# Kernel tuning notes

Hardware: AMD Instinct MI355X
Metric: run time of the kernel (lower is better)

The kernel has to match this reference:

```python
import jax, jax.numpy as jnp
import numpy as np

# regular 3x3 kernel grid: row0 = dy (i-1), row1 = dx (j-1), k = 3*i + j
RY = jnp.array([-1., -1., -1., 0., 0., 0., 1., 1., 1.], dtype=jnp.float32)
RX = jnp.array([-1., 0., 1., -1., 0., 1., -1., 0., 1.], dtype=jnp.float32)


def conv2d(x, w, b):
    # 3x3, stride 1, pad 1, NCHW/OIHW
    out = jax.lax.conv_general_dilated(
        x, w, window_strides=(1, 1), padding=((1, 1), (1, 1)),
        dimension_numbers=('NCHW', 'OIHW', 'NCHW'))
    return out + b[None, :, None, None]


def group_norm(x, gamma, beta, num_groups, eps=1e-5):
    N, C, H, W = x.shape
    xg = x.reshape(N, num_groups, C // num_groups, H, W)
    mu = xg.mean(axis=(2, 3, 4), keepdims=True)
    var = xg.var(axis=(2, 3, 4), keepdims=True)
    xn = ((xg - mu) * jax.lax.rsqrt(var + eps)).reshape(N, C, H, W)
    return xn * gamma[None, :, None, None] + beta[None, :, None, None]


def build_offset(tm, tr):
    # tm: [N,4,H,W] per-pixel 2x2 affine [[m00,m01],[m10,m11]]; tr: [N,2,H,W] (ty, tx)
    m00, m01, m10, m11 = tm[:, 0], tm[:, 1], tm[:, 2], tm[:, 3]  # [N,H,W]
    ry = RY[None, :, None, None]
    rx = RX[None, :, None, None]
    # offset = M @ R - R, plus translation broadcast to all 9 points
    dy = m00[:, None] * ry + m01[:, None] * rx - ry + tr[:, 0:1]  # [N,9,H,W]
    dx = m10[:, None] * ry + m11[:, None] * rx - rx + tr[:, 1:2]  # [N,9,H,W]
    return dy, dx


def bilinear_sample(img, py, px):
    # img: [N,C,H,W]; py, px: [N,K,H,W] sampling locations; zero padding outside
    N, C, H, W = img.shape
    K = py.shape[1]
    y0f = jnp.floor(py)
    x0f = jnp.floor(px)
    wy1 = py - y0f
    wx1 = px - x0f
    wy0 = 1.0 - wy1
    wx0 = 1.0 - wx1
    y0 = y0f.astype(jnp.int32)
    x0 = x0f.astype(jnp.int32)
    img_flat = img.reshape(N, C, H * W)

    def gather(yi, xi):
        valid = ((yi >= 0) & (yi < H) & (xi >= 0) & (xi < W)).astype(img.dtype)
        idx = jnp.clip(yi, 0, H - 1) * W + jnp.clip(xi, 0, W - 1)  # [N,K,H,W]
        flat = idx.reshape(N, 1, K * H * W)
        vals = jnp.take_along_axis(img_flat, jnp.broadcast_to(flat, (N, C, K * H * W)), axis=2)
        return vals.reshape(N, C, K, H, W) * valid[:, None]

    v00 = gather(y0, x0)
    v01 = gather(y0, x0 + 1)
    v10 = gather(y0 + 1, x0)
    v11 = gather(y0 + 1, x0 + 1)
    return (v00 * (wy0 * wx0)[:, None] + v01 * (wy0 * wx1)[:, None]
            + v10 * (wy1 * wx0)[:, None] + v11 * (wy1 * wx1)[:, None])


def deform_conv(x, dy, dx, w, pad=1, dil=1):
    # x: [N,Cin,H,W]; dy,dx: [N,9,H,W]; w: [Cout,Cin,3,3]; stride 1
    N, C, H, W = x.shape
    k = jnp.arange(9)
    ki = (k // 3).astype(x.dtype)[None, :, None, None]
    kj = (k % 3).astype(x.dtype)[None, :, None, None]
    hh = jnp.arange(H, dtype=x.dtype)[None, None, :, None]
    ww = jnp.arange(W, dtype=x.dtype)[None, None, None, :]
    py = hh - pad + dil * ki + dy  # [N,9,H,W]
    px = ww - pad + dil * kj + dx
    sampled = bilinear_sample(x, py, px)  # [N,C,9,H,W]
    return jnp.einsum('nckhw,ock->nohw', sampled, w.reshape(w.shape[0], C, 9))


def setup_inputs() -> dict:
    key = jax.random.key(0)
    ks = jax.random.split(key, 16)
    N, C, H, W = 4, 256, 64, 64
    x = jax.random.normal(ks[0], (N, C, H, W), jnp.float32)
    def p(k, shape, s):
        return jax.random.normal(k, shape, jnp.float32) * s
    s_off = 0.01                       # small STN heads -> modest offsets
    s_dc = 1.0 / np.sqrt(C * 9.0)      # deform-conv fan-in init
    return {
        'x': x,
        'w_tm1': p(ks[1], (4, C, 3, 3), s_off), 'b_tm1': jnp.zeros((4,), jnp.float32),
        'w_tr1': p(ks[2], (2, C, 3, 3), s_off), 'b_tr1': jnp.zeros((2,), jnp.float32),
        'w_dc1': p(ks[3], (C, C, 3, 3), s_dc),
        'g1': jnp.ones((C,), jnp.float32), 'be1': jnp.zeros((C,), jnp.float32),
        'w_tm2': p(ks[4], (4, C, 3, 3), s_off), 'b_tm2': jnp.zeros((4,), jnp.float32),
        'w_tr2': p(ks[5], (2, C, 3, 3), s_off), 'b_tr2': jnp.zeros((2,), jnp.float32),
        'w_dc2': p(ks[6], (C, C, 3, 3), s_dc),
        'g2': jnp.ones((C,), jnp.float32), 'be2': jnp.zeros((C,), jnp.float32),
    }


def reference(x, w_tm1, b_tm1, w_tr1, b_tr1, w_dc1, g1, be1,
              w_tm2, b_tm2, w_tr2, b_tr2, w_dc2, g2, be2):
    GROUPS = 32
    residual = x
    dy1, dx1 = build_offset(conv2d(x, w_tm1, b_tm1), conv2d(x, w_tr1, b_tr1))
    out = deform_conv(x, dy1, dx1, w_dc1)
    out = jax.nn.relu(group_norm(out, g1, be1, GROUPS))
    dy2, dx2 = build_offset(conv2d(out, w_tm2, b_tm2), conv2d(out, w_tr2, b_tr2))
    out = deform_conv(out, dy2, dx2, w_dc2)
    out = group_norm(out, g2, be2, GROUPS)
    return jax.nn.relu(out + residual)
```

## Files before the change

### kernel.cpp

```cpp
#include <hip/hip_runtime.h>


typedef unsigned int u32;
typedef unsigned short u16;
typedef __attribute__((ext_vector_type(8))) short bf16x8;
typedef __attribute__((ext_vector_type(4))) float floatx4;

#define HW 4096
#define CHW 1048576

static __device__ __forceinline__ float bf2f(u16 u) {
    union { u32 i; float f; } c; c.i = ((u32)u) << 16; return c.f;
}
static __device__ __forceinline__ u16 f2bf(float f) {
    union { float f; u32 i; } c; c.f = f;
    u32 x = c.i;
    return (u16)((x + 0x7FFFu + ((x >> 16) & 1u)) >> 16);
}
static __device__ __forceinline__ float loadv(const void* p, long i, int f32) {
    return f32 ? ((const float*)p)[i] : bf2f(((const u16*)p)[i]);
}
static __device__ __forceinline__ int sniff_f32(const u32* __restrict__ xw) {
    int cnt = 0;
    #pragma unroll
    for (int s = 0; s < 16; ++s) {
        union { u32 i; float f; } c;
        c.i = xw[s * 131 + 7];
        float a = fabsf(c.f);
        if (a > 1e-8f && a < 1e4f) ++cnt;
    }
    return (cnt >= 8) ? 1 : 0;
}

__global__ __launch_bounds__(256) void k_prep_all(
    const void* __restrict__ x,
    const void* __restrict__ wdc1, const void* __restrict__ wdc2,
    const void* __restrict__ wtm1, const void* __restrict__ wtr1,
    const void* __restrict__ wtm2, const void* __restrict__ wtr2,
    u16* __restrict__ xT, u16* __restrict__ wTg1, u16* __restrict__ wTg2,
    u16* __restrict__ wT61, u16* __restrict__ wT62)
{
    __shared__ u16 T[64 * 258];
    const int f32 = sniff_f32((const u32*)x);
    const int b = blockIdx.x;
    const int tid = threadIdx.x;

    if (b < 256) {
        const int n = b >> 6, h = b & 63;
        const long sb = (long)n * CHW + (h << 6);
        const int cb = tid >> 3;
        const int w0 = (tid & 7) << 3;
        if (f32) {
            const float* xp = (const float*)x;
            for (int it = 0; it < 8; ++it) {
                int c = (it << 5) + cb;
                const float* pr = xp + sb + (long)c * HW + w0;
                float4 a = ((const float4*)pr)[0];
                float4 d = ((const float4*)pr)[1];
                T[(w0 + 0) * 258 + c] = f2bf(a.x);
                T[(w0 + 1) * 258 + c] = f2bf(a.y);
                T[(w0 + 2) * 258 + c] = f2bf(a.z);
                T[(w0 + 3) * 258 + c] = f2bf(a.w);
                T[(w0 + 4) * 258 + c] = f2bf(d.x);
                T[(w0 + 5) * 258 + c] = f2bf(d.y);
                T[(w0 + 6) * 258 + c] = f2bf(d.z);
                T[(w0 + 7) * 258 + c] = f2bf(d.w);
            }
        } else {
            const u16* xp = (const u16*)x;
            for (int it = 0; it < 8; ++it) {
                int c = (it << 5) + cb;
                uint4 v = *(const uint4*)(xp + sb + (long)c * HW + w0);
                u32 ws[4] = {v.x, v.y, v.z, v.w};
                #pragma unroll
                for (int q = 0; q < 4; ++q) {
                    T[(w0 + 2 * q + 0) * 258 + c] = (u16)(ws[q] & 0xFFFFu);
                    T[(w0 + 2 * q + 1) * 258 + c] = (u16)(ws[q] >> 16);
                }
            }
        }
        __syncthreads();
        const int w = tid >> 2, cq = tid & 3;
        const u32* Tr = (const u32*)T;
        u16* ob = xT + (long)n * CHW + (long)((h << 6) + w) * 256 + cq * 64;
        #pragma unroll
        for (int s = 0; s < 8; ++s) {
            uint4 o;
            o.x = Tr[129 * w + 32 * cq + 4 * s + 0];
            o.y = Tr[129 * w + 32 * cq + 4 * s + 1];
            o.z = Tr[129 * w + 32 * cq + 4 * s + 2];
            o.w = Tr[129 * w + 32 * cq + 4 * s + 3];
            *(uint4*)&ob[s * 8] = o;
        }
    } else if (b < 2560) {
        const int r2 = (b >= 1408);
        const void* wdc = r2 ? wdc2 : wdc1;
        u16* wTg = r2 ? wTg2 : wTg1;
        int idx2 = (b - (r2 ? 1408 : 256)) * 256 + tid;
        int cp = idx2 & 15;
        int o  = (idx2 >> 4) & 255;
        int q  = idx2 >> 12;
        int k  = q >> 3;
        int c0 = ((q & 7) << 5) + (cp << 1);
        long s0 = (long)o * 2304 + c0 * 9 + k;
        u16 w0 = f2bf(loadv(wdc, s0, f32));
        u16 w1 = f2bf(loadv(wdc, s0 + 9, f32));
        ((u32*)wTg)[idx2] = (u32)w0 | ((u32)w1 << 16);
    } else {
        const int r2 = (b >= 2704);
        const void* wtm = r2 ? wtm2 : wtm1;
        const void* wtr = r2 ? wtr2 : wtr1;
        u16* wT6 = r2 ? wT62 : wT61;
        int i = (b - (r2 ? 2704 : 2560)) * 256 + tid;
        int q  = i >> 9;
        int o  = (i >> 5) & 15;
        int cc = i & 31;
        int k  = q >> 3;
        int c  = ((q & 7) << 5) + cc;
        float v = 0.f;
        if (o < 4)      v = loadv(wtm, (long)o * 2304 + c * 9 + k, f32);
        else if (o < 6) v = loadv(wtr, (long)(o - 4) * 2304 + c * 9 + k, f32);
        wT6[i] = f2bf(v);
    }
}

__global__ __launch_bounds__(512, 4) void k_deform(
    const u16* __restrict__ srcT, const u16* __restrict__ wTg,
    const u16* __restrict__ wT6,
    const void* __restrict__ b_tm, const void* __restrict__ b_tr,
    const u32* __restrict__ xw,
    u16* __restrict__ raw, float* __restrict__ pstats)
{
    __shared__ float red[8][32][17];
    __shared__ float tl[6 * 32];
    __shared__ __align__(16) short Sl[2][32 * 40];
    __shared__ int   g_y0[288];
    __shared__ int   g_x0[288];
    __shared__ float g_wy[288];
    __shared__ float g_wx[288];

    const int tid = threadIdx.x;
    const int bid = blockIdx.x;
    const int n = bid >> 7, h = (bid >> 1) & 63, half = bid & 1;
    const int wb = half << 5;
    const int lane = tid & 63;
    const int quad = lane >> 4;
    const int l16  = lane & 15;
    const int wv   = tid >> 6;
    const long nbase = (long)n * CHW;
    const u16* sp = srcT + nbase;

    {
        floatx4 acc6[2];
        acc6[0] = (floatx4){0.f, 0.f, 0.f, 0.f};
        acc6[1] = (floatx4){0.f, 0.f, 0.f, 0.f};
        for (int qi = 0; qi < 9; ++qi) {
            const int q = wv * 9 + qi;
            const int k = q >> 3, cb = q & 7;
            const int ky = k / 3, kx = k % 3;
            const int row = h + ky - 1;
            const bool rv = (row >= 0) && (row < 64);
            bf16x8 av = *(const bf16x8*)&wT6[(((q << 4) + l16) << 5) + (quad << 3)];
            #pragma unroll
            for (int j = 0; j < 2; ++j) {
                int psrc = wb + (j << 4) + l16 + kx - 1;
                bf16x8 bv = {0, 0, 0, 0, 0, 0, 0, 0};
                if (rv && psrc >= 0 && psrc < 64)
                    bv = *(const bf16x8*)&sp[(((long)(row << 6) + psrc) << 8) + (cb << 5) + (quad << 3)];
                acc6[j] = __builtin_amdgcn_mfma_f32_16x16x32_bf16(av, bv, acc6[j], 0, 0, 0);
            }
        }
        #pragma unroll
        for (int j = 0; j < 2; ++j)
            #pragma unroll
            for (int r = 0; r < 4; ++r)
                red[wv][(j << 4) + l16][(quad << 2) + r] = acc6[j][r];
        __syncthreads();
        if (tid < 192) {
            const int o = tid >> 5, px = tid & 31;
            float s = 0.f;
            #pragma unroll
            for (int v = 0; v < 8; ++v) s += red[v][px][o];
            const int f32 = sniff_f32(xw);
            float bias = (o < 4) ? loadv(b_tm, o, f32) : loadv(b_tr, o - 4, f32);
            tl[o * 32 + px] = s + bias;
        }
        __syncthreads();
    }

    for (int i = tid; i < 288; i += 512) {
        int k = i >> 5, ww2 = i & 31;
        float m00 = tl[ww2],       m01 = tl[32 + ww2];
        float m10 = tl[64 + ww2],  m11 = tl[96 + ww2];
        float tr0 = tl[128 + ww2], tr1 = tl[160 + ww2];
        float ry = (float)(k / 3) - 1.f;
        float rx = (float)(k % 3) - 1.f;
        float dy = m00 * ry + m01 * rx - ry + tr0;
        float dx = m10 * ry + m11 * rx - rx + tr1;
        float py = (float)h + ry + dy;
        float px = (float)(wb + ww2) + rx + dx;
        float y0f = floorf(py), x0f = floorf(px);
        g_y0[i] = (int)y0f; g_x0[i] = (int)x0f;
        g_wy[i] = py - y0f; g_wx[i] = px - x0f;
    }
    __syncthreads();

    const int sw  = tid >> 4;
    const int scq = tid & 15;
    const int o0  = wv << 5;

    floatx4 acc[2][2];
    #pragma unroll
    for (int i = 0; i < 2; ++i)
        #pragma unroll
        for (int j = 0; j < 2; ++j)
            acc[i][j] = (floatx4){0.f, 0.f, 0.f, 0.f};

    int a00 = 0, a01 = 0, a10 = 0, a11 = 0;
    float cw00 = 0.f, cw01 = 0.f, cw10 = 0.f, cw11 = 0.f;
    int cur_k = -1;
    u32 s00 = 0, s01 = 0, s10 = 0, s11 = 0;
    bf16x8 wa = {0,0,0,0,0,0,0,0}, wbv = {0,0,0,0,0,0,0,0};

    auto issue = [&](int q) {
        const int k = q >> 3;
        if (k != cur_k) {
            cur_k = k;
            int gi = (k << 5) + sw;
            int y0 = g_y0[gi], x0 = g_x0[gi];
            float wy1 = g_wy[gi], wx1 = g_wx[gi];
            float wy0 = 1.f - wy1, wx0 = 1.f - wx1;
            bool yv0 = (y0 >= 0) && (y0 < 64);
            bool yv1 = (y0 >= -1) && (y0 < 63);
            bool xv0 = (x0 >= 0) && (x0 < 64);
            bool xv1 = (x0 >= -1) && (x0 < 63);
            int yc0 = min(max(y0, 0), 63),     yc1 = min(max(y0 + 1, 0), 63);
            int xc0 = min(max(x0, 0), 63),     xc1 = min(max(x0 + 1, 0), 63);
            a00 = yc0 * 64 + xc0; a01 = yc0 * 64 + xc1;
            a10 = yc1 * 64 + xc0; a11 = yc1 * 64 + xc1;
            cw00 = (yv0 && xv0) ? wy0 * wx0 : 0.f;
            cw01 = (yv0 && xv1) ? wy0 * wx1 : 0.f;
            cw10 = (yv1 && xv0) ? wy1 * wx0 : 0.f;
            cw11 = (yv1 && xv1) ? wy1 * wx1 : 0.f;
        }
        const int cc = ((q & 7) << 5) + (scq << 1);
        s00 = *(const u32*)&sp[(long)a00 * 256 + cc];
        s01 = *(const u32*)&sp[(long)a01 * 256 + cc];
        s10 = *(const u32*)&sp[(long)a10 * 256 + cc];
        s11 = *(const u32*)&sp[(long)a11 * 256 + cc];
        const u16* wp = wTg + (((size_t)q * 256 + o0 + l16) << 5) + (quad << 3);
        wa  = *(const bf16x8*)wp;
        wbv = *(const bf16x8*)(wp + (16 << 5));
    };
    auto publish = [&](int b) {
        float va = fmaf(cw00, bf2f((u16)s00),
                   fmaf(cw01, bf2f((u16)s01),
                   fmaf(cw10, bf2f((u16)s10), cw11 * bf2f((u16)s11))));
        float vb = fmaf(cw00, bf2f((u16)(s00 >> 16)),
                   fmaf(cw01, bf2f((u16)(s01 >> 16)),
                   fmaf(cw10, bf2f((u16)(s10 >> 16)), cw11 * bf2f((u16)(s11 >> 16)))));
        *(u32*)&Sl[b][sw * 40 + (scq << 1)] = (u32)f2bf(va) | ((u32)f2bf(vb) << 16);
    };

    issue(0);
    publish(0);
    bf16x8 A0 = wa, A1 = wbv;
    __syncthreads();

    for (int q = 0; q < 72; ++q) {
        if (q + 1 < 72) issue(q + 1);
        {
            const int b = q & 1;
            #pragma unroll
            for (int j = 0; j < 2; ++j) {
                bf16x8 bv = *(const bf16x8*)&Sl[b][((j << 4) + l16) * 40 + (quad << 3)];
                acc[0][j] = __builtin_amdgcn_mfma_f32_16x16x32_bf16(A0, bv, acc[0][j], 0, 0, 0);
                acc[1][j] = __builtin_amdgcn_mfma_f32_16x16x32_bf16(A1, bv, acc[1][j], 0, 0, 0);
            }
        }
        if (q + 1 < 72) { publish((q + 1) & 1); A0 = wa; A1 = wbv; }
        __syncthreads();
    }

    #pragma unroll
    for (int i = 0; i < 2; ++i) {
        float s1 = 0.f, s2 = 0.f;
        #pragma unroll
        for (int j = 0; j < 2; ++j)
            #pragma unroll
            for (int r = 0; r < 4; ++r) {
                float v = acc[i][j][r];
                s1 += v; s2 += v * v;
            }
        #pragma unroll
        for (int off = 1; off <= 16; off <<= 1) {
            s1 += __shfl_xor(s1, off, 64);
            s2 += __shfl_xor(s2, off, 64);
        }
        if ((lane & 31) == 0) {
            int g = (o0 >> 3) + 2 * i + (lane >> 5);
            pstats[((long)bid << 6) + (g << 1)]     = s1;
            pstats[((long)bid << 6) + (g << 1) + 1] = s2;
        }
    }

    #pragma unroll
    for (int i = 0; i < 2; ++i)
        #pragma unroll
        for (int j = 0; j < 2; ++j)
            #pragma unroll
            for (int r = 0; r < 4; ++r) {
                int o = o0 + i * 16 + quad * 4 + r;
                raw[nbase + ((long)o << 12) + (h << 6) + wb + (j << 4) + l16]
                    = f2bf(acc[i][j][r]);
            }
}

__global__ __launch_bounds__(256) void k_gn_relu(
    const u16* __restrict__ raw, const float* __restrict__ pstats,
    const void* __restrict__ gamma, const void* __restrict__ beta,
    const u32* __restrict__ xw,
    u16* __restrict__ out1)
{
    __shared__ u16 T[64 * 258];
    __shared__ float sred[4][64];
    __shared__ float sl[64];
    const int f32 = sniff_f32(xw);
    const int bid = blockIdx.x;
    const int n = bid >> 6, h = bid & 63;
    const int tid = threadIdx.x;

    {
        const int v = tid & 63, part = tid >> 6;
        float a = 0.f;
        for (int j = part * 32; j < part * 32 + 32; ++j)
            a += pstats[(((long)n * 128 + j) << 6) + v];
        sred[part][v] = a;
        __syncthreads();
        if (tid < 64) sl[tid] = sred[0][tid] + sred[1][tid] + sred[2][tid] + sred[3][tid];
        __syncthreads();
    }

    const u16* rb = raw + (long)n * CHW + (h << 6);
    const int cb = tid >> 3;
    const int w0 = (tid & 7) << 3;
    for (int it = 0; it < 8; ++it) {
        int c = (it << 5) + cb;
        int g = c >> 3;
        float mean = sl[g * 2] * (1.f / 32768.f);
        float var  = sl[g * 2 + 1] * (1.f / 32768.f) - mean * mean;
        float rstd = rsqrtf(var + 1e-5f);
        float ga = loadv(gamma, c, f32) * rstd;
        float be = loadv(beta, c, f32) - mean * ga;
        uint4 v = *(const uint4*)(rb + (long)c * HW + w0);
        u32 ws[4] = {v.x, v.y, v.z, v.w};
        #pragma unroll
        for (int q = 0; q < 4; ++q) {
            float a = fmaxf(fmaf(bf2f((u16)(ws[q] & 0xFFFFu)), ga, be), 0.f);
            float b = fmaxf(fmaf(bf2f((u16)(ws[q] >> 16)),     ga, be), 0.f);
            T[(w0 + 2 * q + 0) * 258 + c] = f2bf(a);
            T[(w0 + 2 * q + 1) * 258 + c] = f2bf(b);
        }
    }
    __syncthreads();
    const int w = tid >> 2, cq = tid & 3;
    const u32* Tr = (const u32*)T;
    u16* ob = out1 + (long)n * CHW + (long)((h << 6) + w) * 256 + cq * 64;
    #pragma unroll
    for (int s = 0; s < 8; ++s) {
        uint4 o;
        o.x = Tr[129 * w + 32 * cq + 4 * s + 0];
        o.y = Tr[129 * w + 32 * cq + 4 * s + 1];
        o.z = Tr[129 * w + 32 * cq + 4 * s + 2];
        o.w = Tr[129 * w + 32 * cq + 4 * s + 3];
        *(uint4*)&ob[s * 8] = o;
    }
}

__global__ __launch_bounds__(256) void k_gn_final(
    const u16* __restrict__ raw, const float* __restrict__ pstats,
    const void* __restrict__ gamma, const void* __restrict__ beta,
    const void* __restrict__ x,
    void* __restrict__ outp)
{
    __shared__ float rr[256];
    const int f32 = sniff_f32((const u32*)x);
    const int tid = threadIdx.x;
    const long e0 = ((long)blockIdx.x) << 11;
    const int n = (int)(e0 >> 20);
    const int c0 = (int)((e0 >> 12) & 255);
    const int g = c0 >> 3;

    {
        int j = tid & 127, sv = tid >> 7;
        rr[tid] = pstats[(((long)n * 128 + j) << 6) + (g << 1) + sv];
        __syncthreads();
        #pragma unroll
        for (int s = 64; s >= 1; s >>= 1) {
            if ((tid & 127) < s) rr[tid] += rr[tid + s];
            __syncthreads();
        }
    }
    float mean = rr[0] * (1.f / 32768.f);
    float var  = rr[128] * (1.f / 32768.f) - mean * mean;
    float rstd = rsqrtf(var + 1e-5f);

    const long i = blockIdx.x * 256 + tid;
    const long e = i << 3;
    const int c = (int)((e >> 12) & 255);
    float ga = loadv(gamma, c, f32) * rstd;
    float be = loadv(beta, c, f32) - mean * ga;
    uint4 p = ((const uint4*)raw)[i];
    u32 ww[4] = {p.x, p.y, p.z, p.w};
    float v[8];
    #pragma unroll
    for (int q = 0; q < 4; ++q) {
        v[2 * q + 0] = fmaxf(fmaf(bf2f((u16)(ww[q] & 0xFFFFu)), ga, be) + loadv(x, e + 2 * q + 0, f32), 0.f);
        v[2 * q + 1] = fmaxf(fmaf(bf2f((u16)(ww[q] >> 16)),     ga, be) + loadv(x, e + 2 * q + 1, f32), 0.f);
    }
    if (f32) {
        float4* op = (float4*)((float*)outp + e);
        op[0] = make_float4(v[0], v[1], v[2], v[3]);
        op[1] = make_float4(v[4], v[5], v[6], v[7]);
    } else {
        uint4 o;
        o.x = (u32)f2bf(v[0]) | ((u32)f2bf(v[1]) << 16);
        o.y = (u32)f2bf(v[2]) | ((u32)f2bf(v[3]) << 16);
        o.z = (u32)f2bf(v[4]) | ((u32)f2bf(v[5]) << 16);
        o.w = (u32)f2bf(v[6]) | ((u32)f2bf(v[7]) << 16);
        ((uint4*)outp)[i] = o;
    }
}

extern "C" void kernel_launch(void* const* d_in, const int* in_sizes, int n_in,
                              void* d_out, int out_size, void* d_ws, size_t ws_size,
                              hipStream_t stream) {
    const void* x     = d_in[0];
    const void* w_tm1 = d_in[1];
    const void* b_tm1 = d_in[2];
    const void* w_tr1 = d_in[3];
    const void* b_tr1 = d_in[4];
    const void* w_dc1 = d_in[5];
    const void* g1    = d_in[6];
    const void* be1   = d_in[7];
    const void* w_tm2 = d_in[8];
    const void* b_tm2 = d_in[9];
    const void* w_tr2 = d_in[10];
    const void* b_tr2 = d_in[11];
    const void* w_dc2 = d_in[12];
    const void* g2    = d_in[13];
    const void* be2   = d_in[14];

    char* wsb = (char*)d_ws;
    u16*   xT     = (u16*)wsb;
    u16*   raw    = (u16*)(wsb + 8388608);
    u16*   wTg1   = (u16*)(wsb + 16777216);
    u16*   wTg2   = (u16*)(wsb + 17956864);
    u16*   wT61   = (u16*)(wsb + 19136512);
    u16*   wT62   = (u16*)(wsb + 19210240);
    float* pstats = (float*)(wsb + 19283968);
    u16*   out1   = xT;
    const u32* xw = (const u32*)x;

    k_prep_all<<<2848, 256, 0, stream>>>(x, w_dc1, w_dc2, w_tm1, w_tr1, w_tm2, w_tr2,
                                         xT, wTg1, wTg2, wT61, wT62);
    k_deform  <<<512, 512, 0, stream>>>(xT, wTg1, wT61, b_tm1, b_tr1, xw, raw, pstats);
    k_gn_relu <<<256, 256, 0, stream>>>(raw, pstats, g1, be1, xw, out1);
    k_deform  <<<512, 512, 0, stream>>>(out1, wTg2, wT62, b_tm2, b_tr2, xw, raw, pstats);
    k_gn_final<<<2048, 256, 0, stream>>>(raw, pstats, g2, be2, x, d_out);
}
```

Baseline: 251.6 us.

## Deepen deform-conv gather pipeline to two stages and use packed bf16 convert

The deformable-conv main loop is restructured so the bilinear gather loads run two K-steps ahead and the weight fragments are double-buffered, unrolled by two. The goal is to hide global gather latency behind MFMA work. Address computation and bilinear-weight computation are now split and cached separately per kernel tap. The manual bf16 rounding is also replaced with the hardware v_cvt_pk_bf16_f32 instruction in several places. The extra in-flight registers raise register pressure and may lower occupancy.

```diff
diff --git a/kernel.cpp b/kernel.cpp
--- a/kernel.cpp
+++ b/kernel.cpp
@@ -16,6 +16,11 @@
     union { float f; u32 i; } c; c.f = f;
     u32 x = c.i;
     return (u16)((x + 0x7FFFu + ((x >> 16) & 1u)) >> 16);
+}
+static __device__ __forceinline__ u32 cvtpk(float a, float b) {
+    u32 r;
+    asm("v_cvt_pk_bf16_f32 %0, %1, %2" : "=v"(r) : "v"(a), "v"(b));
+    return r;
 }
 static __device__ __forceinline__ float loadv(const void* p, long i, int f32) {
     return f32 ? ((const float*)p)[i] : bf2f(((const u16*)p)[i]);
@@ -103,9 +108,7 @@
         int k  = q >> 3;
         int c0 = ((q & 7) << 5) + (cp << 1);
         long s0 = (long)o * 2304 + c0 * 9 + k;
-        u16 w0 = f2bf(loadv(wdc, s0, f32));
-        u16 w1 = f2bf(loadv(wdc, s0 + 9, f32));
-        ((u32*)wTg)[idx2] = (u32)w0 | ((u32)w1 << 16);
+        ((u32*)wTg)[idx2] = cvtpk(loadv(wdc, s0, f32), loadv(wdc, s0 + 9, f32));
     } else {
         const int r2 = (b >= 2704);
         const void* wtm = r2 ? wtm2 : wtm1;
@@ -216,69 +219,88 @@
         for (int j = 0; j < 2; ++j)
             acc[i][j] = (floatx4){0.f, 0.f, 0.f, 0.f};
 
+    int ld_k = -1;
     int a00 = 0, a01 = 0, a10 = 0, a11 = 0;
+    int pb_k = -1;
     float cw00 = 0.f, cw01 = 0.f, cw10 = 0.f, cw11 = 0.f;
-    int cur_k = -1;
-    u32 s00 = 0, s01 = 0, s10 = 0, s11 = 0;
-    bf16x8 wa = {0,0,0,0,0,0,0,0}, wbv = {0,0,0,0,0,0,0,0};
-
-    auto issue = [&](int q) {
-        const int k = q >> 3;
-        if (k != cur_k) {
-            cur_k = k;
-            int gi = (k << 5) + sw;
-            int y0 = g_y0[gi], x0 = g_x0[gi];
-            float wy1 = g_wy[gi], wx1 = g_wx[gi];
-            float wy0 = 1.f - wy1, wx0 = 1.f - wx1;
-            bool yv0 = (y0 >= 0) && (y0 < 64);
-            bool yv1 = (y0 >= -1) && (y0 < 63);
-            bool xv0 = (x0 >= 0) && (x0 < 64);
-            bool xv1 = (x0 >= -1) && (x0 < 63);
-            int yc0 = min(max(y0, 0), 63),     yc1 = min(max(y0 + 1, 0), 63);
-            int xc0 = min(max(x0, 0), 63),     xc1 = min(max(x0 + 1, 0), 63);
-            a00 = yc0 * 64 + xc0; a01 = yc0 * 64 + xc1;
-            a10 = yc1 * 64 + xc0; a11 = yc1 * 64 + xc1;
-            cw00 = (yv0 && xv0) ? wy0 * wx0 : 0.f;
-            cw01 = (yv0 && xv1) ? wy0 * wx1 : 0.f;
-            cw10 = (yv1 && xv0) ? wy1 * wx0 : 0.f;
-            cw11 = (yv1 && xv1) ? wy1 * wx1 : 0.f;
-        }
+
+    auto ld_addr = [&](int k) {
+        int gi = (k << 5) + sw;
+        int y0 = g_y0[gi], x0 = g_x0[gi];
+        int yc0 = min(max(y0, 0), 63),     yc1 = min(max(y0 + 1, 0), 63);
+        int xc0 = min(max(x0, 0), 63),     xc1 = min(max(x0 + 1, 0), 63);
+        a00 = yc0 * 64 + xc0; a01 = yc0 * 64 + xc1;
+        a10 = yc1 * 64 + xc0; a11 = yc1 * 64 + xc1;
+    };
+    auto pb_w = [&](int k) {
+        int gi = (k << 5) + sw;
+        int y0 = g_y0[gi], x0 = g_x0[gi];
+        float wy1 = g_wy[gi], wx1 = g_wx[gi];
+        float wy0 = 1.f - wy1, wx0 = 1.f - wx1;
+        bool yv0 = (y0 >= 0) && (y0 < 64);
+        bool yv1 = (y0 >= -1) && (y0 < 63);
+        bool xv0 = (x0 >= 0) && (x0 < 64);
+        bool xv1 = (x0 >= -1) && (x0 < 63);
+        cw00 = (yv0 && xv0) ? wy0 * wx0 : 0.f;
+        cw01 = (yv0 && xv1) ? wy0 * wx1 : 0.f;
+        cw10 = (yv1 && xv0) ? wy1 * wx0 : 0.f;
+        cw11 = (yv1 && xv1) ? wy1 * wx1 : 0.f;
+    };
+    auto smp = [&](int q, u32& r00, u32& r01, u32& r10, u32& r11) {
+        int k = q >> 3;
+        if (k != ld_k) { ld_k = k; ld_addr(k); }
         const int cc = ((q & 7) << 5) + (scq << 1);
-        s00 = *(const u32*)&sp[(long)a00 * 256 + cc];
-        s01 = *(const u32*)&sp[(long)a01 * 256 + cc];
-        s10 = *(const u32*)&sp[(long)a10 * 256 + cc];
-        s11 = *(const u32*)&sp[(long)a11 * 256 + cc];
+        r00 = *(const u32*)&sp[(long)a00 * 256 + cc];
+        r01 = *(const u32*)&sp[(long)a01 * 256 + cc];
+        r10 = *(const u32*)&sp[(long)a10 * 256 + cc];
+        r11 = *(const u32*)&sp[(long)a11 * 256 + cc];
+    };
+    auto wload = [&](int q, bf16x8& W0, bf16x8& W1) {
         const u16* wp = wTg + (((size_t)q * 256 + o0 + l16) << 5) + (quad << 3);
-        wa  = *(const bf16x8*)wp;
-        wbv = *(const bf16x8*)(wp + (16 << 5));
-    };
-    auto publish = [&](int b) {
-        float va = fmaf(cw00, bf2f((u16)s00),
-                   fmaf(cw01, bf2f((u16)s01),
-                   fmaf(cw10, bf2f((u16)s10), cw11 * bf2f((u16)s11))));
-        float vb = fmaf(cw00, bf2f((u16)(s00 >> 16)),
-                   fmaf(cw01, bf2f((u16)(s01 >> 16)),
-                   fmaf(cw10, bf2f((u16)(s10 >> 16)), cw11 * bf2f((u16)(s11 >> 16)))));
-        *(u32*)&Sl[b][sw * 40 + (scq << 1)] = (u32)f2bf(va) | ((u32)f2bf(vb) << 16);
-    };
-
-    issue(0);
-    publish(0);
-    bf16x8 A0 = wa, A1 = wbv;
+        W0 = *(const bf16x8*)wp;
+        W1 = *(const bf16x8*)(wp + (16 << 5));
+    };
+    auto pub = [&](int q, int b, u32 r00, u32 r01, u32 r10, u32 r11) {
+        int k = q >> 3;
+        if (k != pb_k) { pb_k = k; pb_w(k); }
+        float va = fmaf(cw00, bf2f((u16)r00),
+                   fmaf(cw01, bf2f((u16)r01),
+                   fmaf(cw10, bf2f((u16)r10), cw11 * bf2f((u16)r11))));
+        float vb = fmaf(cw00, bf2f((u16)(r00 >> 16)),
+                   fmaf(cw01, bf2f((u16)(r01 >> 16)),
+                   fmaf(cw10, bf2f((u16)(r10 >> 16)), cw11 * bf2f((u16)(r11 >> 16)))));
+        *(u32*)&Sl[b][sw * 40 + (scq << 1)] = cvtpk(va, vb);
+    };
+    auto mfma4 = [&](int b, bf16x8 W0, bf16x8 W1) {
+        #pragma unroll
+        for (int j = 0; j < 2; ++j) {
+            bf16x8 bv = *(const bf16x8*)&Sl[b][((j << 4) + l16) * 40 + (quad << 3)];
+            acc[0][j] = __builtin_amdgcn_mfma_f32_16x16x32_bf16(W0, bv, acc[0][j], 0, 0, 0);
+            acc[1][j] = __builtin_amdgcn_mfma_f32_16x16x32_bf16(W1, bv, acc[1][j], 0, 0, 0);
+        }
+    };
+
+    u32 sA0, sA1, sA2, sA3, sB0, sB1, sB2, sB3;
+    bf16x8 WA0, WA1, WB0, WB1;
+
+    smp(0, sA0, sA1, sA2, sA3);
+    smp(1, sB0, sB1, sB2, sB3);
+    wload(0, WA0, WA1);
+    wload(1, WB0, WB1);
+    pub(0, 0, sA0, sA1, sA2, sA3);
     __syncthreads();
 
-    for (int q = 0; q < 72; ++q) {
-        if (q + 1 < 72) issue(q + 1);
-        {
-            const int b = q & 1;
-            #pragma unroll
-            for (int j = 0; j < 2; ++j) {
-                bf16x8 bv = *(const bf16x8*)&Sl[b][((j << 4) + l16) * 40 + (quad << 3)];
-                acc[0][j] = __builtin_amdgcn_mfma_f32_16x16x32_bf16(A0, bv, acc[0][j], 0, 0, 0);
-                acc[1][j] = __builtin_amdgcn_mfma_f32_16x16x32_bf16(A1, bv, acc[1][j], 0, 0, 0);
-            }
-        }
-        if (q + 1 < 72) { publish((q + 1) & 1); A0 = wa; A1 = wbv; }
+    for (int q = 0; q < 72; q += 2) {
+        if (q + 2 < 72) smp(q + 2, sA0, sA1, sA2, sA3);
+        mfma4(0, WA0, WA1);
+        pub(q + 1, 1, sB0, sB1, sB2, sB3);
+        if (q + 2 < 72) wload(q + 2, WA0, WA1);
+        __syncthreads();
+
+        if (q + 3 < 72) smp(q + 3, sB0, sB1, sB2, sB3);
+        mfma4(1, WB0, WB1);
+        if (q + 2 < 72) pub(q + 2, 0, sA0, sA1, sA2, sA3);
+        if (q + 3 < 72) wload(q + 3, WB0, WB1);
         __syncthreads();
     }
 
@@ -424,10 +446,10 @@
         op[1] = make_float4(v[4], v[5], v[6], v[7]);
     } else {
         uint4 o;
-        o.x = (u32)f2bf(v[0]) | ((u32)f2bf(v[1]) << 16);
-        o.y = (u32)f2bf(v[2]) | ((u32)f2bf(v[3]) << 16);
-        o.z = (u32)f2bf(v[4]) | ((u32)f2bf(v[5]) << 16);
-        o.w = (u32)f2bf(v[6]) | ((u32)f2bf(v[7]) << 16);
+        o.x = cvtpk(v[0], v[1]);
+        o.y = cvtpk(v[2], v[3]);
+        o.z = cvtpk(v[4], v[5]);
+        o.w = cvtpk(v[6], v[7]);
         ((uint4*)outp)[i] = o;
     }
 }
```

Result: no change. 249.6 us (-0.8%).
